# Optimization experiments

Hardware: AMD Instinct MI355X
Metric: run time of the kernel (lower is better)

Reference implementation:

```python
import jax, jax.numpy as jnp
import numpy as np

B, N, T, D, H = 8, 64, 256, 256, 8
HD = D // H


def _mlp(x, W1, b1, W2, b2):
    # torch nn.Sequential(Linear, GELU(exact), Linear); weights stored pre-transposed
    return jax.nn.gelu(x @ W1 + b1, approximate=False) @ W2 + b2


def setup_inputs() -> dict:
    key = jax.random.key(0)
    ks = jax.random.split(key, 14)
    s = 0.02
    f32 = jnp.float32
    return {
        "padded_batches": jax.random.normal(ks[0], (B, N, T, D), f32),
        "sum_token": jax.random.normal(ks[1], (B, N, 1, D), f32),
        "masks": jax.random.randint(ks[2], (B, N, T), 0, 2).astype(jnp.int32),
        "positions_3d": jax.random.normal(ks[3], (B, N, T, 3), f32),
        "Wq": jax.random.normal(ks[4], (D, D), f32) * s, "bq": jnp.zeros((D,), f32),
        "Wk": jax.random.normal(ks[5], (D, D), f32) * s, "bk": jnp.zeros((D,), f32),
        "Wv": jax.random.normal(ks[6], (D, D), f32) * s, "bv": jnp.zeros((D,), f32),
        "Bw1": jax.random.normal(ks[7], (5, 64), f32) * s, "Bb1": jnp.zeros((64,), f32),
        "Bw2": jax.random.normal(ks[8], (64, H), f32) * s, "Bb2": jnp.zeros((H,), f32),
        "Vw1": jax.random.normal(ks[9], (5, 128), f32) * s, "Vb1": jnp.zeros((128,), f32),
        "Vw2": jax.random.normal(ks[10], (128, D), f32) * s, "Vb2": jnp.zeros((D,), f32),
    }


def reference(padded_batches, sum_token, masks, positions_3d,
              Wq, bq, Wk, bk, Wv, bv,
              Bw1, Bb1, Bw2, Bb2, Vw1, Vb1, Vw2, Vb2):
    Bd, Nd, Td, Dd = padded_batches.shape
    BN = Bd * Nd
    # masked-average summary token (summary_mode='avg'): [B,N,1,D]
    w = masks[..., None].astype(padded_batches.dtype)            # [B,N,T,1]
    denom = jnp.clip(w.sum(-2, keepdims=True), 1e-6)
    summary = (padded_batches * w).sum(-2, keepdims=True) / denom
    # projections (torch Linear: x @ W.T + b; weights here pre-transposed)
    q = (padded_batches @ Wq + bq).reshape(BN, Td, H, HD).transpose(0, 2, 1, 3)  # [BN,H,T,Hd]
    k = (summary @ Wk + bk).reshape(BN, 1, H, HD).transpose(0, 2, 1, 3)          # [BN,H,1,Hd]
    v = (summary @ Wv + bv).reshape(BN, 1, H, HD).transpose(0, 2, 1, 3)
    scale = 1.0 / np.sqrt(HD).astype(np.float32)
    logits = jnp.einsum('bhtd,bhsd->bhts', q, k) * scale          # [BN,H,T,1]
    # relative positional features vs. position summary
    pos_summary = (positions_3d * w).sum(-2, keepdims=True) / denom  # [B,N,1,3]
    diff = positions_3d.reshape(BN, Td, 1, 3) - pos_summary.reshape(BN, 1, 1, 3)  # [BN,T,1,3]
    dist = jnp.linalg.norm(diff, axis=-1, keepdims=True)
    dist2 = (diff ** 2).sum(-1, keepdims=True)
    rel_feat = jnp.concatenate([diff, dist, dist2], axis=-1)      # [BN,T,1,5]
    rel_bias = _mlp(rel_feat, Bw1, Bb1, Bw2, Bb2).transpose(0, 3, 1, 2)  # [BN,H,T,1]
    logits = logits + rel_bias
    neg = jnp.finfo(jnp.float32).min
    attn_mask = jnp.where(masks.reshape(BN, 1, Td, 1) == 0, neg, 0.0)
    logits = logits + attn_mask
    attn_w = jax.nn.softmax(logits, axis=-1)                      # [BN,H,T,1]
    attn = jnp.einsum('bhts,bhsd->bhtd', attn_w, v)               # [BN,H,T,Hd]
    rel_val = _mlp(rel_feat, Vw1, Vb1, Vw2, Vb2)                  # [BN,T,1,D]
    rel_val = rel_val.reshape(BN, Td, 1, H, HD).transpose(0, 3, 1, 2, 4)  # [BN,H,T,1,Hd]
    attn = attn + (attn_w[..., None] * rel_val).sum(-2)
    out = attn.transpose(0, 2, 1, 3).reshape(Bd, Nd, Td, Dd) + padded_batches
    return out
```

## Files before the change

### kernel.cpp

```cpp
#include <hip/hip_runtime.h>
#include <hip/hip_bf16.h>
#include <math.h>


#define BN_TOT 512
#define T_DIM 256
#define D_DIM 256
#define HID 128

typedef __attribute__((ext_vector_type(8))) short short8v;
typedef __attribute__((ext_vector_type(4))) float f32x4;

static __device__ __forceinline__ ushort f2bf(float f) {
    __hip_bfloat16 h = __float2bfloat16(f);
    return *reinterpret_cast<ushort*>(&h);
}

__global__ __launch_bounds__(128) void k_prep(const float* __restrict__ Vw2,
                                              ushort* __restrict__ Vw2t) {
    const int d = blockIdx.x;
    const int k = threadIdx.x;
    Vw2t[d * HID + k] = f2bf(Vw2[k * D_DIM + d]);
}

__global__ __launch_bounds__(512, 8) void k_sum(
    const float* __restrict__ x,
    const int* __restrict__ masks,
    const float* __restrict__ pos,
    const float* __restrict__ Wv,
    const float* __restrict__ bv,
    const float* __restrict__ Vb2,
    float* __restrict__ v_ws,
    float* __restrict__ ps_ws)
{
    __shared__ float s_m[256];
    __shared__ float s_red[4 * 256];
    __shared__ float s_part[8 * 256];
    __shared__ float s_sum[256];

    const int bn = blockIdx.x, tid = threadIdx.x;
    const float* xb = x + (size_t)bn * T_DIM * D_DIM;

    if (tid < 256) {
        float m = (float)masks[bn * T_DIM + tid];
        s_m[tid] = m;
        const float* pp = pos + ((size_t)bn * T_DIM + tid) * 3;
        s_red[0 * 256 + tid] = m;
        s_red[1 * 256 + tid] = m * pp[0];
        s_red[2 * 256 + tid] = m * pp[1];
        s_red[3 * 256 + tid] = m * pp[2];
    }
    __syncthreads();

    {
        const int dq = tid & 63, tq = tid >> 6;
        float4 a = make_float4(0.f, 0.f, 0.f, 0.f);
        const float* px = xb + (size_t)tq * 32 * D_DIM + dq * 4;
        #pragma unroll 8
        for (int i = 0; i < 32; ++i) {
            float m = s_m[tq * 32 + i];
            float4 xv = *reinterpret_cast<const float4*>(px + i * D_DIM);
            a.x += m * xv.x; a.y += m * xv.y; a.z += m * xv.z; a.w += m * xv.w;
        }
        *reinterpret_cast<float4*>(s_part + tq * 256 + dq * 4) = a;
    }
    __syncthreads();

    for (int off = 128; off > 0; off >>= 1) {
        if (tid < off) {
            s_red[0 * 256 + tid] += s_red[0 * 256 + tid + off];
            s_red[1 * 256 + tid] += s_red[1 * 256 + tid + off];
            s_red[2 * 256 + tid] += s_red[2 * 256 + tid + off];
            s_red[3 * 256 + tid] += s_red[3 * 256 + tid + off];
        }
        __syncthreads();
    }
    const float inv = 1.0f / fmaxf(s_red[0], 1e-6f);
    if (tid < 3) ps_ws[bn * 4 + tid] = s_red[(tid + 1) * 256] * inv;

    if (tid < 256) {
        float s = 0.f;
        #pragma unroll
        for (int q = 0; q < 8; ++q) s += s_part[q * 256 + tid];
        s_sum[tid] = s * inv;
    }
    __syncthreads();

    {
        const int dq = tid & 63, kq = tid >> 6;
        float4 a = make_float4(0.f, 0.f, 0.f, 0.f);
        #pragma unroll 8
        for (int i = 0; i < 32; ++i) {
            const int k = kq * 32 + i;
            float sc = s_sum[k];
            float4 w = *reinterpret_cast<const float4*>(Wv + (size_t)k * D_DIM + dq * 4);
            a.x += sc * w.x; a.y += sc * w.y; a.z += sc * w.z; a.w += sc * w.w;
        }
        *reinterpret_cast<float4*>(s_part + kq * 256 + dq * 4) = a;
    }
    __syncthreads();
    if (tid < 256) {
        float r = bv[tid] + Vb2[tid];
        #pragma unroll
        for (int q = 0; q < 8; ++q) r += s_part[q * 256 + tid];
        v_ws[bn * D_DIM + tid] = r;
    }
}

__global__ __launch_bounds__(256, 4) void k_main(
    const float* __restrict__ x,
    const float* __restrict__ pos,
    const float* __restrict__ Vw1,
    const float* __restrict__ Vb1,
    const ushort* __restrict__ Vw2t,
    const float* __restrict__ v_ws,
    const float* __restrict__ ps_ws,
    float* __restrict__ out)
{
    __shared__ float s_rf[64 * 6];
    __shared__ float s_w1[5 * 128];
    __shared__ float s_b1[128];
    __shared__ float s_vb[256];
    __shared__ unsigned char s_hid[64 * HID * 2];

    const int tg  = blockIdx.x;
    const int bn  = blockIdx.y;
    const int tid = threadIdx.x;
    const int t0  = tg * 64;

    s_vb[tid] = v_ws[bn * D_DIM + tid];
    if (tid < 256) {  }
    for (int i = tid; i < 640; i += 256) s_w1[i] = Vw1[i];
    if (tid < 128) s_b1[tid] = Vb1[tid];

    const float psx = ps_ws[bn * 4 + 0];
    const float psy = ps_ws[bn * 4 + 1];
    const float psz = ps_ws[bn * 4 + 2];
    if (tid < 64) {
        const float* pp = pos + ((size_t)bn * T_DIM + t0 + tid) * 3;
        float dx = pp[0] - psx, dy = pp[1] - psy, dz = pp[2] - psz;
        float d2 = dx * dx + dy * dy + dz * dz;
        s_rf[tid * 6 + 0] = dx; s_rf[tid * 6 + 1] = dy; s_rf[tid * 6 + 2] = dz;
        s_rf[tid * 6 + 3] = sqrtf(d2); s_rf[tid * 6 + 4] = d2;
    }
    __syncthreads();

    {
        const int cg = tid & 15;
        const int c0 = cg * 8;
        float wv[5][8], bb[8];
        #pragma unroll
        for (int e = 0; e < 5; ++e)
            #pragma unroll
            for (int j = 0; j < 8; ++j) wv[e][j] = s_w1[e * HID + c0 + j];
        #pragma unroll
        for (int j = 0; j < 8; ++j) bb[j] = s_b1[c0 + j];

        #pragma unroll
        for (int s = 0; s < 4; ++s) {
            const int tok = (tid >> 4) + s * 16;
            const float* rf = s_rf + tok * 6;
            const float dx = rf[0], dy = rf[1], dz = rf[2], dd = rf[3], d2 = rf[4];
            uint pk[4];
            #pragma unroll
            for (int jj = 0; jj < 4; ++jj) {
                float g[2];
                #pragma unroll
                for (int h = 0; h < 2; ++h) {
                    const int j = jj * 2 + h;
                    float z = bb[j] + dx * wv[0][j] + dy * wv[1][j] + dz * wv[2][j]
                                    + dd * wv[3][j] + d2 * wv[4][j];
                    g[h] = 0.5f * z * (1.0f + erff(z * 0.70710678118654752f));
                }
                pk[jj] = (uint)f2bf(g[0]) | ((uint)f2bf(g[1]) << 16);
            }
            int byte = tok * 256 + cg * 16;
            byte ^= (tok & 15) << 4;
            *reinterpret_cast<uint4*>(s_hid + byte) = make_uint4(pk[0], pk[1], pk[2], pk[3]);
        }
    }
    __syncthreads();

    const int l  = tid & 63;
    const int wc = tid >> 6;

    f32x4 acc[4][4];
    #pragma unroll
    for (int m = 0; m < 4; ++m)
        #pragma unroll
        for (int n = 0; n < 4; ++n) acc[m][n] = (f32x4){0.f, 0.f, 0.f, 0.f};

    const ushort* bbase = Vw2t + ((size_t)(wc * 64 + (l & 15))) * HID + ((l >> 4) * 8);
    const int koff16 = (l >> 4) * 16;

    #pragma unroll
    for (int ks = 0; ks < 4; ++ks) {
        short8v wfr[4];
        #pragma unroll
        for (int n = 0; n < 4; ++n)
            wfr[n] = *reinterpret_cast<const short8v*>(bbase + n * 16 * HID + ks * 32);
        short8v hfr[4];
        #pragma unroll
        for (int m = 0; m < 4; ++m) {
            const int tok = m * 16 + (l & 15);
            int byte = tok * 256 + ks * 64 + koff16;
            byte ^= (tok & 15) << 4;
            hfr[m] = *reinterpret_cast<const short8v*>(s_hid + byte);
        }
        #pragma unroll
        for (int m = 0; m < 4; ++m)
            #pragma unroll
            for (int n = 0; n < 4; ++n)
                acc[m][n] = __builtin_amdgcn_mfma_f32_16x16x32_bf16(
                    wfr[n], hfr[m], acc[m][n], 0, 0, 0);
    }

    #pragma unroll
    for (int m = 0; m < 4; ++m) {
        const int tok = m * 16 + (l & 15);
        const float* xr   = x   + ((size_t)bn * T_DIM + t0 + tok) * D_DIM;
        float*       orow = out + ((size_t)bn * T_DIM + t0 + tok) * D_DIM;
        #pragma unroll
        for (int n = 0; n < 4; ++n) {
            const int d0 = wc * 64 + n * 16 + ((l >> 4) << 2);
            float4 xv  = *reinterpret_cast<const float4*>(xr + d0);
            float4 vb4 = *reinterpret_cast<const float4*>(s_vb + d0);
            float4 o;
            o.x = xv.x + vb4.x + acc[m][n][0];
            o.y = xv.y + vb4.y + acc[m][n][1];
            o.z = xv.z + vb4.z + acc[m][n][2];
            o.w = xv.w + vb4.w + acc[m][n][3];
            *reinterpret_cast<float4*>(orow + d0) = o;
        }
    }
}

extern "C" void kernel_launch(void* const* d_in, const int* in_sizes, int n_in,
                              void* d_out, int out_size, void* d_ws, size_t ws_size,
                              hipStream_t stream) {
    const float* x     = (const float*)d_in[0];
    const int*   masks = (const int*)d_in[2];
    const float* pos   = (const float*)d_in[3];
    const float* Wv    = (const float*)d_in[8];
    const float* bv    = (const float*)d_in[9];
    const float* Vw1   = (const float*)d_in[14];
    const float* Vb1   = (const float*)d_in[15];
    const float* Vw2   = (const float*)d_in[16];
    const float* Vb2   = (const float*)d_in[17];
    float* out = (float*)d_out;

    ushort* Vw2t = (ushort*)d_ws;
    float*  v_ws = (float*)(Vw2t + D_DIM * HID);
    float*  ps_ws = v_ws + BN_TOT * D_DIM;

    k_prep<<<D_DIM, HID, 0, stream>>>(Vw2, Vw2t);
    k_sum<<<BN_TOT, 512, 0, stream>>>(x, masks, pos, Wv, bv, Vb2, v_ws, ps_ws);
    k_main<<<dim3(4, BN_TOT), 256, 0, stream>>>(x, pos, Vw1, Vb1, Vw2t,
                                                v_ws, ps_ws, out);
}
```

Before: 97.16 us.

## Split masked summary reduction across more blocks and halve main-kernel token tile

Replaces the single-block-per-sequence summary reduction with a two-stage scheme. k_part computes masked partial sums over 64-token chunks (2048 blocks), and k_v combines them and applies Wv. The original k_sum is kept as a fallback when the workspace is too small. k_main now processes 32 tokens per block over 8 tiles instead of 64 over 4, and k_prep writes packed ushort4 outputs. The goal is more parallelism and better occupancy, at the cost of an extra launch, extra partial-sum traffic through global memory, and reloading the MLP weights in twice as many main blocks.

Measured after the change: 106.2 us. 9.3% more time.

```diff
diff --git a/kernel.cpp b/kernel.cpp
--- a/kernel.cpp
+++ b/kernel.cpp
@@ -16,22 +16,120 @@
     return *reinterpret_cast<ushort*>(&h);
 }
 
-__global__ __launch_bounds__(128) void k_prep(const float* __restrict__ Vw2,
+__global__ __launch_bounds__(256) void k_prep(const float* __restrict__ Vw2,
                                               ushort* __restrict__ Vw2t) {
-    const int d = blockIdx.x;
-    const int k = threadIdx.x;
-    Vw2t[d * HID + k] = f2bf(Vw2[k * D_DIM + d]);
-}
-
-__global__ __launch_bounds__(512, 8) void k_sum(
+    const int idx = (blockIdx.x * 256 + threadIdx.x) * 4;
+    const int d = idx >> 7, k = idx & 127;
+    ushort4 r;
+    r.x = f2bf(Vw2[(size_t)(k + 0) * D_DIM + d]);
+    r.y = f2bf(Vw2[(size_t)(k + 1) * D_DIM + d]);
+    r.z = f2bf(Vw2[(size_t)(k + 2) * D_DIM + d]);
+    r.w = f2bf(Vw2[(size_t)(k + 3) * D_DIM + d]);
+    *reinterpret_cast<ushort4*>(Vw2t + d * HID + k) = r;
+}
+
+__global__ __launch_bounds__(256, 8) void k_part(
     const float* __restrict__ x,
     const int* __restrict__ masks,
     const float* __restrict__ pos,
+    float* __restrict__ part_x,
+    float* __restrict__ part_cp)
+{
+    __shared__ float s_part[4 * 256];
+
+    const int bid = blockIdx.x;
+    const int tid = threadIdx.x;
+    const int bn = bid >> 2, tg = bid & 3;
+    const int t0 = tg * 64;
+
+    const float* xb = x + ((size_t)bn * T_DIM + t0) * D_DIM;
+    const int*   mb = masks + bn * T_DIM + t0;
+
+    {
+        const int dq = tid & 63, tq = tid >> 6;
+        float4 a = make_float4(0.f, 0.f, 0.f, 0.f);
+        #pragma unroll
+        for (int i = 0; i < 16; ++i) {
+            const int t = tq * 16 + i;
+            float m = (float)mb[t];
+            float4 xv = *reinterpret_cast<const float4*>(xb + (size_t)t * D_DIM + dq * 4);
+            a.x += m * xv.x; a.y += m * xv.y; a.z += m * xv.z; a.w += m * xv.w;
+        }
+        *reinterpret_cast<float4*>(s_part + tq * 256 + dq * 4) = a;
+    }
+
+    if (tid < 64) {
+        float m = (float)mb[tid];
+        const float* pp = pos + ((size_t)bn * T_DIM + t0 + tid) * 3;
+        float c = m, px = m * pp[0], py = m * pp[1], pz = m * pp[2];
+        #pragma unroll
+        for (int off = 32; off > 0; off >>= 1) {
+            c  += __shfl_down(c,  off, 64);
+            px += __shfl_down(px, off, 64);
+            py += __shfl_down(py, off, 64);
+            pz += __shfl_down(pz, off, 64);
+        }
+        if (tid == 0)
+            *reinterpret_cast<float4*>(part_cp + (bn * 4 + tg) * 4) =
+                make_float4(c, px, py, pz);
+    }
+    __syncthreads();
+
+    float s = s_part[tid] + s_part[256 + tid] + s_part[512 + tid] + s_part[768 + tid];
+    part_x[((size_t)bn * 4 + tg) * 256 + tid] = s;
+}
+
+__global__ __launch_bounds__(256, 8) void k_v(
+    const float* __restrict__ part_x,
+    const float* __restrict__ part_cp,
     const float* __restrict__ Wv,
     const float* __restrict__ bv,
     const float* __restrict__ Vb2,
     float* __restrict__ v_ws,
     float* __restrict__ ps_ws)
+{
+    __shared__ float s_sum[256];
+    __shared__ float s_part[4 * 256];
+    __shared__ float s_cp[16];
+
+    const int bn = blockIdx.x, tid = threadIdx.x;
+
+    if (tid < 16) s_cp[tid] = part_cp[bn * 16 + tid];
+    const float* pb = part_x + (size_t)bn * 1024;
+    float s = pb[tid] + pb[256 + tid] + pb[512 + tid] + pb[768 + tid];
+    __syncthreads();
+
+    const float cnt = s_cp[0] + s_cp[4] + s_cp[8] + s_cp[12];
+    const float inv = 1.0f / fmaxf(cnt, 1e-6f);
+    s_sum[tid] = s * inv;
+    if (tid < 3) {
+        float p = s_cp[tid + 1] + s_cp[tid + 5] + s_cp[tid + 9] + s_cp[tid + 13];
+        ps_ws[bn * 4 + tid] = p * inv;
+    }
+    __syncthreads();
+
+    {
+        const int dq = tid & 63, kq = tid >> 6;
+        float4 a = make_float4(0.f, 0.f, 0.f, 0.f);
+        #pragma unroll 8
+        for (int i = 0; i < 64; ++i) {
+            const int k = kq * 64 + i;
+            float sc = s_sum[k];
+            float4 w = *reinterpret_cast<const float4*>(Wv + (size_t)k * D_DIM + dq * 4);
+            a.x += sc * w.x; a.y += sc * w.y; a.z += sc * w.z; a.w += sc * w.w;
+        }
+        *reinterpret_cast<float4*>(s_part + kq * 256 + dq * 4) = a;
+    }
+    __syncthreads();
+    v_ws[bn * D_DIM + tid] = s_part[tid] + s_part[256 + tid] + s_part[512 + tid] +
+                             s_part[768 + tid] + bv[tid] + Vb2[tid];
+}
+
+__global__ __launch_bounds__(512, 8) void k_sum(
+    const float* __restrict__ x, const int* __restrict__ masks,
+    const float* __restrict__ pos, const float* __restrict__ Wv,
+    const float* __restrict__ bv, const float* __restrict__ Vb2,
+    float* __restrict__ v_ws, float* __restrict__ ps_ws)
 {
     __shared__ float s_m[256];
     __shared__ float s_red[4 * 256];
@@ -51,7 +149,6 @@
         s_red[3 * 256 + tid] = m * pp[2];
     }
     __syncthreads();
-
     {
         const int dq = tid & 63, tq = tid >> 6;
         float4 a = make_float4(0.f, 0.f, 0.f, 0.f);
@@ -65,7 +162,6 @@
         *reinterpret_cast<float4*>(s_part + tq * 256 + dq * 4) = a;
     }
     __syncthreads();
-
     for (int off = 128; off > 0; off >>= 1) {
         if (tid < off) {
             s_red[0 * 256 + tid] += s_red[0 * 256 + tid + off];
@@ -77,7 +173,6 @@
     }
     const float inv = 1.0f / fmaxf(s_red[0], 1e-6f);
     if (tid < 3) ps_ws[bn * 4 + tid] = s_red[(tid + 1) * 256] * inv;
-
     if (tid < 256) {
         float s = 0.f;
         #pragma unroll
@@ -85,7 +180,6 @@
         s_sum[tid] = s * inv;
     }
     __syncthreads();
-
     {
         const int dq = tid & 63, kq = tid >> 6;
         float4 a = make_float4(0.f, 0.f, 0.f, 0.f);
@@ -117,26 +211,25 @@
     const float* __restrict__ ps_ws,
     float* __restrict__ out)
 {
-    __shared__ float s_rf[64 * 6];
+    __shared__ float s_rf[32 * 6];
     __shared__ float s_w1[5 * 128];
     __shared__ float s_b1[128];
     __shared__ float s_vb[256];
-    __shared__ unsigned char s_hid[64 * HID * 2];
+    __shared__ unsigned char s_hid[32 * HID * 2];
 
     const int tg  = blockIdx.x;
     const int bn  = blockIdx.y;
     const int tid = threadIdx.x;
-    const int t0  = tg * 64;
+    const int t0  = tg * 32;
 
     s_vb[tid] = v_ws[bn * D_DIM + tid];
-    if (tid < 256) {  }
     for (int i = tid; i < 640; i += 256) s_w1[i] = Vw1[i];
     if (tid < 128) s_b1[tid] = Vb1[tid];
 
     const float psx = ps_ws[bn * 4 + 0];
     const float psy = ps_ws[bn * 4 + 1];
     const float psz = ps_ws[bn * 4 + 2];
-    if (tid < 64) {
+    if (tid < 32) {
         const float* pp = pos + ((size_t)bn * T_DIM + t0 + tid) * 3;
         float dx = pp[0] - psx, dy = pp[1] - psy, dz = pp[2] - psz;
         float d2 = dx * dx + dy * dy + dz * dz;
@@ -157,7 +250,7 @@
         for (int j = 0; j < 8; ++j) bb[j] = s_b1[c0 + j];
 
         #pragma unroll
-        for (int s = 0; s < 4; ++s) {
+        for (int s = 0; s < 2; ++s) {
             const int tok = (tid >> 4) + s * 16;
             const float* rf = s_rf + tok * 6;
             const float dx = rf[0], dy = rf[1], dz = rf[2], dd = rf[3], d2 = rf[4];
@@ -184,9 +277,9 @@
     const int l  = tid & 63;
     const int wc = tid >> 6;
 
-    f32x4 acc[4][4];
+    f32x4 acc[2][4];
     #pragma unroll
-    for (int m = 0; m < 4; ++m)
+    for (int m = 0; m < 2; ++m)
         #pragma unroll
         for (int n = 0; n < 4; ++n) acc[m][n] = (f32x4){0.f, 0.f, 0.f, 0.f};
 
@@ -199,16 +292,16 @@
         #pragma unroll
         for (int n = 0; n < 4; ++n)
             wfr[n] = *reinterpret_cast<const short8v*>(bbase + n * 16 * HID + ks * 32);
-        short8v hfr[4];
-        #pragma unroll
-        for (int m = 0; m < 4; ++m) {
+        short8v hfr[2];
+        #pragma unroll
+        for (int m = 0; m < 2; ++m) {
             const int tok = m * 16 + (l & 15);
             int byte = tok * 256 + ks * 64 + koff16;
             byte ^= (tok & 15) << 4;
             hfr[m] = *reinterpret_cast<const short8v*>(s_hid + byte);
         }
         #pragma unroll
-        for (int m = 0; m < 4; ++m)
+        for (int m = 0; m < 2; ++m)
             #pragma unroll
             for (int n = 0; n < 4; ++n)
                 acc[m][n] = __builtin_amdgcn_mfma_f32_16x16x32_bf16(
@@ -216,7 +309,7 @@
     }
 
     #pragma unroll
-    for (int m = 0; m < 4; ++m) {
+    for (int m = 0; m < 2; ++m) {
         const int tok = m * 16 + (l & 15);
         const float* xr   = x   + ((size_t)bn * T_DIM + t0 + tok) * D_DIM;
         float*       orow = out + ((size_t)bn * T_DIM + t0 + tok) * D_DIM;
@@ -249,12 +342,20 @@
     const float* Vb2   = (const float*)d_in[17];
     float* out = (float*)d_out;
 
-    ushort* Vw2t = (ushort*)d_ws;
-    float*  v_ws = (float*)(Vw2t + D_DIM * HID);
+    ushort* Vw2t  = (ushort*)d_ws;
+    float*  v_ws  = (float*)(Vw2t + D_DIM * HID);
     float*  ps_ws = v_ws + BN_TOT * D_DIM;
-
-    k_prep<<<D_DIM, HID, 0, stream>>>(Vw2, Vw2t);
-    k_sum<<<BN_TOT, 512, 0, stream>>>(x, masks, pos, Wv, bv, Vb2, v_ws, ps_ws);
-    k_main<<<dim3(4, BN_TOT), 256, 0, stream>>>(x, pos, Vw1, Vb1, Vw2t,
+    float*  part_x  = ps_ws + BN_TOT * 4;
+    float*  part_cp = part_x + (size_t)BN_TOT * 4 * 256;
+    const size_t need_main = (size_t)(part_cp + BN_TOT * 16 - (float*)d_ws) * 4;
+
+    k_prep<<<32, 256, 0, stream>>>(Vw2, Vw2t);
+    if (ws_size >= need_main) {
+        k_part<<<BN_TOT * 4, 256, 0, stream>>>(x, masks, pos, part_x, part_cp);
+        k_v<<<BN_TOT, 256, 0, stream>>>(part_x, part_cp, Wv, bv, Vb2, v_ws, ps_ws);
+    } else {
+        k_sum<<<BN_TOT, 512, 0, stream>>>(x, masks, pos, Wv, bv, Vb2, v_ws, ps_ws);
+    }
+    k_main<<<dim3(8, BN_TOT), 256, 0, stream>>>(x, pos, Vw1, Vb1, Vw2t,
                                                 v_ws, ps_ws, out);
 }
```
